# Performance work log

Hardware: AMD Instinct MI355X
Metric: run time of the kernel (lower is better)

## Reference

```python
import jax, jax.numpy as jnp
import numpy as np

N_NODES = 20000
N_EDGES = 500000


def setup_inputs() -> dict:
    key = jax.random.key(0)
    ks = jax.random.split(key, 12)
    s = 0.05  # small init scale for numerical sanity
    return {
        "z": jax.random.normal(ks[0], (N_NODES, 64), jnp.float32),
        "edge_index": jax.random.randint(ks[1], (2, N_EDGES), 0, N_NODES, jnp.int64),
        "celline_feats": jax.random.normal(ks[2], (N_NODES, 4), jnp.float32),
        "esm_repr": jax.random.normal(ks[3], (N_NODES, 320), jnp.float32),
        "mlp_w1": jax.random.normal(ks[4], (4, 64), jnp.float32) * s,
        "mlp_b1": jnp.zeros((64,), jnp.float32),
        "mlp_w2": jax.random.normal(ks[5], (64, 32), jnp.float32) * s,
        "mlp_b2": jnp.zeros((32,), jnp.float32),
        "mlp_w3": jax.random.normal(ks[6], (32, 16), jnp.float32) * s,
        "mlp_b3": jnp.zeros((16,), jnp.float32),
        "fc1_w": jax.random.normal(ks[7], (800, 400), jnp.float32) * s,
        "fc1_b": jnp.zeros((400,), jnp.float32),
        "fc2_w": jax.random.normal(ks[8], (400, 200), jnp.float32) * s,
        "fc2_b": jnp.zeros((200,), jnp.float32),
        "fc3_w": jax.random.normal(ks[9], (200, 100), jnp.float32) * s,
        "fc3_b": jnp.zeros((100,), jnp.float32),
        "fc4_w": jax.random.normal(ks[10], (100, 1), jnp.float32) * s,
        "fc4_b": jnp.zeros((1,), jnp.float32),
    }


def reference(z, edge_index, celline_feats, esm_repr,
              mlp_w1, mlp_b1, mlp_w2, mlp_b2, mlp_w3, mlp_b3,
              fc1_w, fc1_b, fc2_w, fc2_b, fc3_w, fc3_b, fc4_w, fc4_b):
    # cell_line_spec_mlp: 4 -> 64 -> 32 -> 16 (relu, relu, linear)
    m = jax.nn.relu(celline_feats @ mlp_w1 + mlp_b1)
    m = jax.nn.relu(m @ mlp_w2 + mlp_b2)
    m = m @ mlp_w3 + mlp_b3                       # [N, 16]
    # augment node embeddings: [N, 64+16+320] = [N, 400]
    zc = jnp.concatenate([z, m, esm_repr], axis=1)
    # gather endpoints, concat pair features: [E, 800]
    x = jnp.concatenate([zc[edge_index[0]], zc[edge_index[1]]], axis=1)
    # classifier MLP (dropout = identity in eval mode)
    x = jax.nn.relu(x @ fc1_w + fc1_b)
    x = jax.nn.relu(x @ fc2_w + fc2_b)
    x = jax.nn.relu(x @ fc3_w + fc3_b)
    x = x @ fc4_w + fc4_b                          # [E, 1]
    return jnp.squeeze(x, axis=-1)                 # [E]
```

## Files before the change

### kernel.cpp

```cpp
#include <hip/hip_runtime.h>


using u16    = unsigned short;
using f16    = _Float16;
using f16x8  = __attribute__((ext_vector_type(8))) f16;
using f32x4  = __attribute__((ext_vector_type(4))) float;
using f32x16 = __attribute__((ext_vector_type(16))) float;
using i32x4  = __attribute__((ext_vector_type(4))) int;

#define NN   20000
#define NNP  20032
#define KD   416
#define NE   500000
#define NEP  500736
#define GRID_E 3912
#define NB   157

#define W1F_ELEMS (50*13*512)
#define W2F_ELEMS (7*26*512)
#define W3F_ELEMS (4*14*512)
#define F4_ELEMS  128
#define PREP_TOT  (W1F_ELEMS + W2F_ELEMS + W3F_ELEMS + F4_ELEMS)

#define ZC_BLOCKS   (NNP / 4)
#define PREP_BLOCKS ((PREP_TOT + 255) / 256)
#define HIST_BLOCKS ((NE + 1023) / 1024)

__device__ __forceinline__ u16 f2h(float f) {
  f16 h = (f16)f;
  return __builtin_bit_cast(u16, h);
}

__device__ __forceinline__ int cvt_pk_f16(float lo, float hi) {
  int r;
  asm("v_cvt_pkrtz_f16_f32 %0, %1, %2" : "=v"(r) : "v"(lo), "v"(hi));
  return r;
}

__device__ __forceinline__ int pk_addrelu(int p, int q) {
  int r;
  asm("v_pk_add_f16 %0, %1, %2\n\t"
      "v_pk_max_f16 %0, %0, 0"
      : "=&v"(r) : "v"(p), "v"(q));
  return r;
}

__device__ __forceinline__ void gl_lds16(const u16* g, u16* l) {
  __builtin_amdgcn_global_load_lds(
      (const __attribute__((address_space(1))) unsigned int*)g,
      (__attribute__((address_space(3))) unsigned int*)l, 16, 0, 0);
}

__global__ __launch_bounds__(256) void prep_fused(
    const float* __restrict__ z, const float* __restrict__ cell,
    const float* __restrict__ esm,
    const float* __restrict__ w1, const float* __restrict__ b1,
    const float* __restrict__ w2, const float* __restrict__ b2,
    const float* __restrict__ w3, const float* __restrict__ b3,
    u16* __restrict__ zc,
    const float* __restrict__ fc1, const float* __restrict__ fc1b,
    const float* __restrict__ fc2, const float* __restrict__ fc2b,
    const float* __restrict__ fc3, const float* __restrict__ fc3b,
    const float* __restrict__ fc4,
    u16* __restrict__ W1f, u16* __restrict__ W2f, u16* __restrict__ W3f,
    float* __restrict__ fc4wp,
    const int* __restrict__ ei, int* __restrict__ hist)
{
  __shared__ float h1s[4][64];
  __shared__ float h2s[4][32];
  __shared__ float ms[4][16];
  __shared__ int lh[NB];

  if (blockIdx.x < ZC_BLOCKS) {
    int tid = threadIdx.x, g = tid >> 6, t = tid & 63;
    int i = blockIdx.x * 4 + g;
    bool real = (i < NN);
    float c0 = 0, c1 = 0, c2 = 0, c3 = 0;
    if (real) {
      c0 = cell[(size_t)i * 4 + 0]; c1 = cell[(size_t)i * 4 + 1];
      c2 = cell[(size_t)i * 4 + 2]; c3 = cell[(size_t)i * 4 + 3];
    }
    float h = b1[t] + c0 * w1[t] + c1 * w1[64 + t] + c2 * w1[128 + t] + c3 * w1[192 + t];
    h1s[g][t] = fmaxf(h, 0.f);
    __syncthreads();
    if (t < 32) {
      float acc = b2[t];
      #pragma unroll 8
      for (int j = 0; j < 64; j++) acc += h1s[g][j] * w2[j * 32 + t];
      h2s[g][t] = fmaxf(acc, 0.f);
    }
    __syncthreads();
    if (t < 16) {
      float acc = b3[t];
      #pragma unroll 8
      for (int j = 0; j < 32; j++) acc += h2s[g][j] * w3[j * 16 + t];
      ms[g][t] = acc;
    }
    __syncthreads();
    u16* row = zc + (size_t)i * KD;
    for (int k = t; k < KD; k += 64) {
      float v = 0.f;
      if (real) {
        if (k < 64)       v = z[(size_t)i * 64 + k];
        else if (k < 80)  v = ms[g][k - 64];
        else if (k < 400) v = esm[(size_t)i * 320 + (k - 80)];
        else if (k == 400) v = 1.0f;
      }
      row[k] = f2h(v);
    }
    return;
  }

  if (blockIdx.x >= ZC_BLOCKS + PREP_BLOCKS) {
    int tid = threadIdx.x;
    int base = (blockIdx.x - (ZC_BLOCKS + PREP_BLOCKS)) * 1024;
    for (int i = tid; i < NB; i += 256) lh[i] = 0;
    __syncthreads();
    #pragma unroll
    for (int k = 0; k < 4; k++) {
      int e = base + k * 256 + tid;
      if (e < NE) atomicAdd(&lh[ei[e] >> 7], 1);
    }
    __syncthreads();
    for (int i = tid; i < NB; i += 256)
      if (lh[i]) atomicAdd(&hist[i], lh[i]);
    return;
  }

  int idx = (blockIdx.x - ZC_BLOCKS) * 256 + threadIdx.x;
  if (idx < W1F_ELEMS) {
    int j = idx & 7, l = (idx >> 3) & 63, t = idx >> 9;
    int kb = t % 13, g = t / 13;
    int n = g * 16 + (l & 15);
    int k = kb * 32 + (l >> 4) * 8 + j;
    float v = 0.f;
    if (k < 400) v = (n < 400) ? fc1[(size_t)k * 400 + n]
                               : fc1[(size_t)(400 + k) * 400 + (n - 400)];
    else if (k == 400 && n < 400) v = fc1b[n];
    W1f[idx] = f2h(v);
  } else if (idx < W1F_ELEMS + W2F_ELEMS) {
    int r = idx - W1F_ELEMS;
    int j = r & 7, l = (r >> 3) & 63, t = r >> 9;
    int kb = t % 26, nt = t / 26;
    int n = nt * 32 + (l & 31);
    int k = kb * 16 + (l >> 5) * 8 + j;
    float v = 0.f;
    if (n < 200) {
      if (k < 400) v = fc2[(size_t)k * 200 + n];
      else if (k == 400) v = fc2b[n];
    }
    W2f[r] = f2h(v);
  } else if (idx < W1F_ELEMS + W2F_ELEMS + W3F_ELEMS) {
    int r = idx - (W1F_ELEMS + W2F_ELEMS);
    int j = r & 7, l = (r >> 3) & 63, t = r >> 9;
    int kb = t % 14, nt = t / 14;
    int n = nt * 32 + (l & 31);
    int k = kb * 16 + (l >> 5) * 8 + j;
    float v = 0.f;
    if (n < 100) {
      if (k < 200) v = fc3[(size_t)k * 100 + n];
      else if (k == 200) v = fc3b[n];
    }
    W3f[r] = f2h(v);
  } else if (idx < PREP_TOT) {
    int r = idx - (W1F_ELEMS + W2F_ELEMS + W3F_ELEMS);
    fc4wp[r] = (r < 100) ? fc4[r] : 0.f;
  }
}

__global__ __launch_bounds__(256) void scan_pad(
    const int* __restrict__ hist, int* __restrict__ cursor,
    int* __restrict__ sq, int* __restrict__ dq, int* __restrict__ oq)
{
  __shared__ int h[NB];
  __shared__ int cs[NB];
  int t = threadIdx.x;
  if (t < NB) h[t] = hist[t];
  __syncthreads();
  if (t == 0) {
    int run = 0;
    for (int b = 0; b < NB; b++) { cs[b] = run; run += h[b]; }
  }
  __syncthreads();
  if (t < NB) cursor[t] = cs[t];
  for (int i = NE + t; i < NEP; i += 256) {
    sq[i] = 0; dq[i] = 0; oq[i] = 0x7FFFFFFF;
  }
}

__global__ __launch_bounds__(256) void scatter_edges(
    const int* __restrict__ ei, int* __restrict__ cursor,
    int* __restrict__ sq, int* __restrict__ dq, int* __restrict__ oq)
{
  __shared__ int lh[NB];
  __shared__ int lb[NB];
  int t = threadIdx.x;
  int base = blockIdx.x * 1024;
  for (int i = t; i < NB; i += 256) lh[i] = 0;
  __syncthreads();
  int sv[4], dv[4], bv[4], rv[4];
  bool val[4];
  #pragma unroll
  for (int k = 0; k < 4; k++) {
    int e = base + k * 256 + t;
    val[k] = (e < NE);
    if (val[k]) {
      sv[k] = ei[e]; dv[k] = ei[NE + e];
      bv[k] = sv[k] >> 7;
      rv[k] = atomicAdd(&lh[bv[k]], 1);
    }
  }
  __syncthreads();
  for (int i = t; i < NB; i += 256)
    lb[i] = lh[i] ? atomicAdd(&cursor[i], lh[i]) : 0;
  __syncthreads();
  #pragma unroll
  for (int k = 0; k < 4; k++) {
    if (val[k]) {
      int pos = lb[bv[k]] + rv[k];
      sq[pos] = sv[k]; dq[pos] = dv[k]; oq[pos] = base + k * 256 + t;
    }
  }
}

__global__ __launch_bounds__(256) void node_gemm(
    const u16* __restrict__ zc, const u16* __restrict__ W1f,
    u16* __restrict__ PQ)
{
  int tid = threadIdx.x, w = tid >> 6, l = tid & 63, lm = l & 15, quad = l >> 4;
  int mbase = blockIdx.x * 128 + w * 32;

  int ra = mbase + lm;       if (ra > NNP - 1) ra = NNP - 1;
  int rb = mbase + 16 + lm;  if (rb > NNP - 1) rb = NNP - 1;
  f16x8 a0[13], a1[13];
  const u16* arow0 = zc + (size_t)ra * KD + quad * 8;
  const u16* arow1 = zc + (size_t)rb * KD + quad * 8;
  #pragma unroll
  for (int kb = 0; kb < 13; kb++) {
    a0[kb] = *(const f16x8*)(arow0 + kb * 32);
    a1[kb] = *(const f16x8*)(arow1 + kb * 32);
  }

  for (int nt = 0; nt < 10; nt++) {
    int g = blockIdx.y * 10 + nt;
    int ncol = g * 16 + lm;
    const u16* bbase = W1f + ((size_t)g * 13 * 64 + l) * 8;
    f32x4 acc0 = {0.f, 0.f, 0.f, 0.f};
    f32x4 acc1 = {0.f, 0.f, 0.f, 0.f};
    #pragma unroll
    for (int kb = 0; kb < 13; kb++) {
      f16x8 b = *(const f16x8*)(bbase + (size_t)kb * 512);
      acc0 = __builtin_amdgcn_mfma_f32_16x16x32_f16(a0[kb], b, acc0, 0, 0, 0);
      acc1 = __builtin_amdgcn_mfma_f32_16x16x32_f16(a1[kb], b, acc1, 0, 0, 0);
    }
    #pragma unroll
    for (int r = 0; r < 4; r++) {
      int row0 = mbase + quad * 4 + r;
      int row1 = row0 + 16;
      if (row0 < NNP) PQ[(size_t)row0 * 800 + ncol] = f2h(acc0[r]);
      if (row1 < NNP) PQ[(size_t)row1 * 800 + ncol] = f2h(acc1[r]);
    }
  }
}

__global__ __launch_bounds__(256, 2) void edge_kernel(
    const u16* __restrict__ PQ, const u16* __restrict__ W2f,
    const u16* __restrict__ W3f, const float* __restrict__ fc4wp,
    const float* __restrict__ fc4b,
    const int* __restrict__ sq, const int* __restrict__ dq,
    const int* __restrict__ oq, float* __restrict__ out)
{
  __shared__ __align__(16) u16 wsm[2][26 * 512];

  int tid = threadIdx.x, w = tid >> 6, l = tid & 63;
  int c = l & 31, h = l >> 5;
  int bid = blockIdx.x;
  int idx = (bid & 7) * (GRID_E / 8) + (bid >> 3);
  int e = idx * 128 + w * 32 + c;
  int s = sq[e], d = dq[e], oi = oq[e];
  const u16* prow = PQ + (size_t)s * 800 + h * 8;
  const u16* qrow = PQ + (size_t)d * 800 + 400 + h * 8;

  for (int kb = w; kb < 26; kb += 4)
    gl_lds16(W2f + ((size_t)kb * 64 + l) * 8, &wsm[0][kb * 512]);

  i32x4 h1i[25];
  #pragma unroll
  for (int kb = 0; kb < 25; kb++) {
    i32x4 pv = *(const i32x4*)(prow + kb * 16);
    i32x4 qv = *(const i32x4*)(qrow + kb * 16);
    i32x4 r;
    #pragma unroll
    for (int j2 = 0; j2 < 4; j2++) r[j2] = pk_addrelu(pv[j2], qv[j2]);
    h1i[kb] = r;
  }
  i32x4 bias1 = {0, 0, 0, 0};
  if (h == 0) bias1[0] = 0x3C00;

  __syncthreads();

  int p2[7][8];
  #pragma unroll
  for (int nt = 0; nt < 7; nt++) {
    int cur = nt & 1;
    if (nt < 6) {
      for (int kb = w; kb < 26; kb += 4)
        gl_lds16(W2f + (((size_t)(nt + 1) * 26 + kb) * 64 + l) * 8,
                 &wsm[cur ^ 1][kb * 512]);
    } else {
      for (int kb = w; kb < 13; kb += 4)
        gl_lds16(W3f + ((size_t)kb * 64 + l) * 8, &wsm[cur ^ 1][kb * 512]);
    }
    f32x16 acc = {0.f,0.f,0.f,0.f,0.f,0.f,0.f,0.f,0.f,0.f,0.f,0.f,0.f,0.f,0.f,0.f};
    __builtin_amdgcn_s_setprio(1);
    #pragma unroll
    for (int kb = 0; kb < 25; kb++) {
      f16x8 a = *(const f16x8*)&wsm[cur][kb * 512 + l * 8];
      acc = __builtin_amdgcn_mfma_f32_32x32x16_f16(
          a, __builtin_bit_cast(f16x8, h1i[kb]), acc, 0, 0, 0);
    }
    {
      f16x8 a = *(const f16x8*)&wsm[cur][25 * 512 + l * 8];
      acc = __builtin_amdgcn_mfma_f32_32x32x16_f16(
          a, __builtin_bit_cast(f16x8, bias1), acc, 0, 0, 0);
    }
    __builtin_amdgcn_s_setprio(0);
    #pragma unroll
    for (int q = 0; q < 8; q++)
      p2[nt][q] = cvt_pk_f16(fmaxf(acc[2 * q], 0.f), fmaxf(acc[2 * q + 1], 0.f));
    __syncthreads();
  }

  i32x4 b2f[13];
  #pragma unroll
  for (int kb3 = 0; kb3 < 13; kb3++) {
    int nt = kb3 >> 1;
    i32x4 f;
    #pragma unroll
    for (int jj = 0; jj < 4; jj++) {
      int q0 = (jj & 1) + 4 * (kb3 & 1);
      if (jj < 2) {
        int x = __shfl_xor(p2[nt][q0 + 2], 32);
        f[jj] = h ? x : p2[nt][q0];
      } else {
        int y = __shfl_xor(p2[nt][q0], 32);
        f[jj] = h ? p2[nt][q0 + 2] : y;
      }
    }
    if (kb3 == 12 && h) f[0] |= 0x3C00;
    b2f[kb3] = f;
  }

  float osum = 0.f;
  #pragma unroll
  for (int nt3 = 0; nt3 < 4; nt3++) {
    int cur = (7 + nt3) & 1;
    if (nt3 < 3) {
      for (int kb = w; kb < 13; kb += 4)
        gl_lds16(W3f + (((size_t)(nt3 + 1) * 14 + kb) * 64 + l) * 8,
                 &wsm[cur ^ 1][kb * 512]);
    }
    f32x16 acc = {0.f,0.f,0.f,0.f,0.f,0.f,0.f,0.f,0.f,0.f,0.f,0.f,0.f,0.f,0.f,0.f};
    __builtin_amdgcn_s_setprio(1);
    #pragma unroll
    for (int kb3 = 0; kb3 < 13; kb3++) {
      f16x8 a = *(const f16x8*)&wsm[cur][kb3 * 512 + l * 8];
      acc = __builtin_amdgcn_mfma_f32_32x32x16_f16(
          a, __builtin_bit_cast(f16x8, b2f[kb3]), acc, 0, 0, 0);
    }
    __builtin_amdgcn_s_setprio(0);
    #pragma unroll
    for (int r = 0; r < 16; r++) {
      int rho = (r & 3) + 8 * (r >> 2) + 4 * h + 32 * nt3;
      osum += fmaxf(acc[r], 0.f) * fc4wp[rho];
    }
    if (nt3 < 3) __syncthreads();
  }
  osum += __shfl_xor(osum, 32);
  if (h == 0 && oi < NE) out[oi] = osum + fc4b[0];
}

extern "C" void kernel_launch(void* const* d_in, const int* in_sizes, int n_in,
                              void* d_out, int out_size, void* d_ws, size_t ws_size,
                              hipStream_t stream) {
  (void)in_sizes; (void)n_in; (void)out_size; (void)ws_size;
  const float* z    = (const float*)d_in[0];
  const int*   ei   = (const int*)d_in[1];
  const float* cell = (const float*)d_in[2];
  const float* esm  = (const float*)d_in[3];
  const float* w1   = (const float*)d_in[4];
  const float* b1   = (const float*)d_in[5];
  const float* w2   = (const float*)d_in[6];
  const float* b2   = (const float*)d_in[7];
  const float* w3   = (const float*)d_in[8];
  const float* b3   = (const float*)d_in[9];
  const float* fc1w = (const float*)d_in[10];
  const float* fc1b = (const float*)d_in[11];
  const float* fc2w = (const float*)d_in[12];
  const float* fc2b = (const float*)d_in[13];
  const float* fc3w = (const float*)d_in[14];
  const float* fc3b = (const float*)d_in[15];
  const float* fc4w = (const float*)d_in[16];
  const float* fc4b = (const float*)d_in[17];
  float* out = (float*)d_out;

  u16* zc  = (u16*)d_ws;
  u16* PQ  = zc  + (size_t)NNP * KD;
  u16* W1f = PQ  + (size_t)NNP * 800;
  u16* W2f = W1f + W1F_ELEMS;
  u16* W3f = W2f + W2F_ELEMS;
  float* fc4wp = (float*)(W3f + W3F_ELEMS);
  int* hist   = (int*)(fc4wp + 128);
  int* cursor = hist + 160;
  int* sq     = cursor + 160;
  int* dq     = sq + NEP;
  int* oq     = dq + NEP;

  hipMemsetAsync(hist, 0, NB * sizeof(int), stream);
  prep_fused<<<ZC_BLOCKS + PREP_BLOCKS + HIST_BLOCKS, 256, 0, stream>>>(
      z, cell, esm, w1, b1, w2, b2, w3, b3, zc,
      fc1w, fc1b, fc2w, fc2b, fc3w, fc3b, fc4w, W1f, W2f, W3f, fc4wp,
      ei, hist);
  scan_pad<<<1, 256, 0, stream>>>(hist, cursor, sq, dq, oq);
  scatter_edges<<<HIST_BLOCKS, 256, 0, stream>>>(ei, cursor, sq, dq, oq);
  node_gemm<<<dim3((NNP + 127) / 128, 5), 256, 0, stream>>>(zc, W1f, PQ);
  edge_kernel<<<GRID_E, 256, 0, stream>>>(PQ, W2f, W3f, fc4wp, fc4b,
                                          sq, dq, oq, out);
}
```

Measured before the change: 370.2 us.

## Split edge-kernel weight staging into half-tile double buffers to halve LDS

Weight tiles for the fc2 and fc3 layers are now staged in halves of the K dimension rather than whole tiles. The double buffer shrinks from two 26-block slots to two 13-block slots. Each output tile computes its first half from one buffer while the second half loads, then swaps after a mid-tile barrier. This halves shared-memory use, which could allow more resident blocks, at the cost of an extra __syncthreads per tile and a shorter window for hiding loads.

Measured after the change: 378.9 us. 2.3% more time.

```diff
diff --git a/kernel.cpp b/kernel.cpp
--- a/kernel.cpp
+++ b/kernel.cpp
@@ -263,6 +263,34 @@
   }
 }
 
+
+#define STAGE2(nt, hf, b) \
+  for (int kb = w; kb < 13; kb += 4) \
+    gl_lds16(W2f + (((size_t)(nt) * 26 + (hf) * 13 + kb) * 64 + l) * 8, \
+             &wsm[b][kb * 512]);
+
+#define STAGE3(nt, hf, b) \
+  for (int kb = w; kb < ((hf) ? 6 : 7); kb += 4) \
+    gl_lds16(W3f + (((size_t)(nt) * 14 + (hf) * 7 + kb) * 64 + l) * 8, \
+             &wsm[b][kb * 512]);
+
+#define FC2_HALF(hf, b) \
+  _Pragma("unroll") \
+  for (int kk = 0; kk < 13; kk++) { \
+    int gkb = (hf) * 13 + kk; \
+    f16x8 a = *(const f16x8*)&wsm[b][kk * 512 + l * 8]; \
+    acc = __builtin_amdgcn_mfma_f32_32x32x16_f16( \
+        a, __builtin_bit_cast(f16x8, gkb < 25 ? h1i[gkb] : bias1), acc, 0, 0, 0); \
+  }
+
+#define FC3_HALF(hf, b) \
+  _Pragma("unroll") \
+  for (int kk = 0; kk < ((hf) ? 6 : 7); kk++) { \
+    f16x8 a = *(const f16x8*)&wsm[b][kk * 512 + l * 8]; \
+    acc = __builtin_amdgcn_mfma_f32_32x32x16_f16( \
+        a, __builtin_bit_cast(f16x8, b2f[(hf) * 7 + kk]), acc, 0, 0, 0); \
+  }
+
 __global__ __launch_bounds__(256, 2) void edge_kernel(
     const u16* __restrict__ PQ, const u16* __restrict__ W2f,
     const u16* __restrict__ W3f, const float* __restrict__ fc4wp,
@@ -270,7 +298,7 @@
     const int* __restrict__ sq, const int* __restrict__ dq,
     const int* __restrict__ oq, float* __restrict__ out)
 {
-  __shared__ __align__(16) u16 wsm[2][26 * 512];
+  __shared__ __align__(16) u16 wsm[2][13 * 512];
 
   int tid = threadIdx.x, w = tid >> 6, l = tid & 63;
   int c = l & 31, h = l >> 5;
@@ -281,8 +309,7 @@
   const u16* prow = PQ + (size_t)s * 800 + h * 8;
   const u16* qrow = PQ + (size_t)d * 800 + 400 + h * 8;
 
-  for (int kb = w; kb < 26; kb += 4)
-    gl_lds16(W2f + ((size_t)kb * 64 + l) * 8, &wsm[0][kb * 512]);
+  STAGE2(0, 0, 0);
 
   i32x4 h1i[25];
   #pragma unroll
@@ -302,28 +329,16 @@
   int p2[7][8];
   #pragma unroll
   for (int nt = 0; nt < 7; nt++) {
-    int cur = nt & 1;
-    if (nt < 6) {
-      for (int kb = w; kb < 26; kb += 4)
-        gl_lds16(W2f + (((size_t)(nt + 1) * 26 + kb) * 64 + l) * 8,
-                 &wsm[cur ^ 1][kb * 512]);
-    } else {
-      for (int kb = w; kb < 13; kb += 4)
-        gl_lds16(W3f + ((size_t)kb * 64 + l) * 8, &wsm[cur ^ 1][kb * 512]);
-    }
+    STAGE2(nt, 1, 1);
     f32x16 acc = {0.f,0.f,0.f,0.f,0.f,0.f,0.f,0.f,0.f,0.f,0.f,0.f,0.f,0.f,0.f,0.f};
     __builtin_amdgcn_s_setprio(1);
-    #pragma unroll
-    for (int kb = 0; kb < 25; kb++) {
-      f16x8 a = *(const f16x8*)&wsm[cur][kb * 512 + l * 8];
-      acc = __builtin_amdgcn_mfma_f32_32x32x16_f16(
-          a, __builtin_bit_cast(f16x8, h1i[kb]), acc, 0, 0, 0);
-    }
-    {
-      f16x8 a = *(const f16x8*)&wsm[cur][25 * 512 + l * 8];
-      acc = __builtin_amdgcn_mfma_f32_32x32x16_f16(
-          a, __builtin_bit_cast(f16x8, bias1), acc, 0, 0, 0);
-    }
+    FC2_HALF(0, 0);
+    __builtin_amdgcn_s_setprio(0);
+    __syncthreads();
+    if (nt < 6) { STAGE2(nt + 1, 0, 0); }
+    else        { STAGE3(0, 0, 0); }
+    __builtin_amdgcn_s_setprio(1);
+    FC2_HALF(1, 1);
     __builtin_amdgcn_s_setprio(0);
     #pragma unroll
     for (int q = 0; q < 8; q++)
@@ -354,20 +369,15 @@
   float osum = 0.f;
   #pragma unroll
   for (int nt3 = 0; nt3 < 4; nt3++) {
-    int cur = (7 + nt3) & 1;
-    if (nt3 < 3) {
-      for (int kb = w; kb < 13; kb += 4)
-        gl_lds16(W3f + (((size_t)(nt3 + 1) * 14 + kb) * 64 + l) * 8,
-                 &wsm[cur ^ 1][kb * 512]);
-    }
+    STAGE3(nt3, 1, 1);
     f32x16 acc = {0.f,0.f,0.f,0.f,0.f,0.f,0.f,0.f,0.f,0.f,0.f,0.f,0.f,0.f,0.f,0.f};
     __builtin_amdgcn_s_setprio(1);
-    #pragma unroll
-    for (int kb3 = 0; kb3 < 13; kb3++) {
-      f16x8 a = *(const f16x8*)&wsm[cur][kb3 * 512 + l * 8];
-      acc = __builtin_amdgcn_mfma_f32_32x32x16_f16(
-          a, __builtin_bit_cast(f16x8, b2f[kb3]), acc, 0, 0, 0);
-    }
+    FC3_HALF(0, 0);
+    __builtin_amdgcn_s_setprio(0);
+    __syncthreads();
+    if (nt3 < 3) { STAGE3(nt3 + 1, 0, 0); }
+    __builtin_amdgcn_s_setprio(1);
+    FC3_HALF(1, 1);
     __builtin_amdgcn_s_setprio(0);
     #pragma unroll
     for (int r = 0; r < 16; r++) {
```

## Bucket edges by 2D source/destination node blocks for gather locality

Applied to the files above, without the earlier changes.

Edges were bucketed by source block only (157 buckets). They are now bucketed by the (source block, destination block) pair, giving 157x157 buckets. The goal is to make the per-edge gathers of PQ rows in the edge kernel hit a small working set of both source and destination nodes, improving cache reuse. In exchange the histogram and scatter use global atomics directly, with no shared-memory aggregation, which adds contention. A single block now scans about 24.6K buckets serially per thread, and the workspace grows.

Result: slower. 433.5 us (+17.1%).

```diff
diff --git a/kernel.cpp b/kernel.cpp
--- a/kernel.cpp
+++ b/kernel.cpp
@@ -14,7 +14,8 @@
 #define NE   500000
 #define NEP  500736
 #define GRID_E 3912
-#define NB   157
+#define NBS  157
+#define NB2  (157*157)
 
 #define W1F_ELEMS (50*13*512)
 #define W2F_ELEMS (7*26*512)
@@ -69,7 +70,6 @@
   __shared__ float h1s[4][64];
   __shared__ float h2s[4][32];
   __shared__ float ms[4][16];
-  __shared__ int lh[NB];
 
   if (blockIdx.x < ZC_BLOCKS) {
     int tid = threadIdx.x, g = tid >> 6, t = tid & 63;
@@ -114,16 +114,14 @@
   if (blockIdx.x >= ZC_BLOCKS + PREP_BLOCKS) {
     int tid = threadIdx.x;
     int base = (blockIdx.x - (ZC_BLOCKS + PREP_BLOCKS)) * 1024;
-    for (int i = tid; i < NB; i += 256) lh[i] = 0;
-    __syncthreads();
     #pragma unroll
     for (int k = 0; k < 4; k++) {
       int e = base + k * 256 + tid;
-      if (e < NE) atomicAdd(&lh[ei[e] >> 7], 1);
-    }
-    __syncthreads();
-    for (int i = tid; i < NB; i += 256)
-      if (lh[i]) atomicAdd(&hist[i], lh[i]);
+      if (e < NE) {
+        int s = ei[e], d = ei[NE + e];
+        atomicAdd(&hist[(s >> 7) * NBS + (d >> 7)], 1);
+      }
+    }
     return;
   }
 
@@ -172,17 +170,21 @@
     const int* __restrict__ hist, int* __restrict__ cursor,
     int* __restrict__ sq, int* __restrict__ dq, int* __restrict__ oq)
 {
-  __shared__ int h[NB];
-  __shared__ int cs[NB];
+  __shared__ int part[256];
   int t = threadIdx.x;
-  if (t < NB) h[t] = hist[t];
+  const int per = (NB2 + 255) / 256;
+  int lo = t * per, hi = lo + per; if (hi > NB2) hi = NB2;
+  int sum = 0;
+  for (int i = lo; i < hi; i++) sum += hist[i];
+  part[t] = sum;
   __syncthreads();
   if (t == 0) {
     int run = 0;
-    for (int b = 0; b < NB; b++) { cs[b] = run; run += h[b]; }
+    for (int i = 0; i < 256; i++) { int v = part[i]; part[i] = run; run += v; }
   }
   __syncthreads();
-  if (t < NB) cursor[t] = cs[t];
+  int run = part[t];
+  for (int i = lo; i < hi; i++) { int v = hist[i]; cursor[i] = run; run += v; }
   for (int i = NE + t; i < NEP; i += 256) {
     sq[i] = 0; dq[i] = 0; oq[i] = 0x7FFFFFFF;
   }
@@ -192,33 +194,16 @@
     const int* __restrict__ ei, int* __restrict__ cursor,
     int* __restrict__ sq, int* __restrict__ dq, int* __restrict__ oq)
 {
-  __shared__ int lh[NB];
-  __shared__ int lb[NB];
   int t = threadIdx.x;
   int base = blockIdx.x * 1024;
-  for (int i = t; i < NB; i += 256) lh[i] = 0;
-  __syncthreads();
-  int sv[4], dv[4], bv[4], rv[4];
-  bool val[4];
   #pragma unroll
   for (int k = 0; k < 4; k++) {
     int e = base + k * 256 + t;
-    val[k] = (e < NE);
-    if (val[k]) {
-      sv[k] = ei[e]; dv[k] = ei[NE + e];
-      bv[k] = sv[k] >> 7;
-      rv[k] = atomicAdd(&lh[bv[k]], 1);
-    }
-  }
-  __syncthreads();
-  for (int i = t; i < NB; i += 256)
-    lb[i] = lh[i] ? atomicAdd(&cursor[i], lh[i]) : 0;
-  __syncthreads();
-  #pragma unroll
-  for (int k = 0; k < 4; k++) {
-    if (val[k]) {
-      int pos = lb[bv[k]] + rv[k];
-      sq[pos] = sv[k]; dq[pos] = dv[k]; oq[pos] = base + k * 256 + t;
+    if (e < NE) {
+      int s = ei[e], d = ei[NE + e];
+      int key = (s >> 7) * NBS + (d >> 7);
+      int pos = atomicAdd(&cursor[key], 1);
+      sq[pos] = s; dq[pos] = d; oq[pos] = e;
     }
   }
 }
@@ -411,12 +396,12 @@
   u16* W3f = W2f + W2F_ELEMS;
   float* fc4wp = (float*)(W3f + W3F_ELEMS);
   int* hist   = (int*)(fc4wp + 128);
-  int* cursor = hist + 160;
-  int* sq     = cursor + 160;
+  int* cursor = hist + NB2;
+  int* sq     = cursor + NB2;
   int* dq     = sq + NEP;
   int* oq     = dq + NEP;
 
-  hipMemsetAsync(hist, 0, NB * sizeof(int), stream);
+  hipMemsetAsync(hist, 0, NB2 * sizeof(int), stream);
   prep_fused<<<ZC_BLOCKS + PREP_BLOCKS + HIST_BLOCKS, 256, 0, stream>>>(
       z, cell, esm, w1, b1, w2, b2, w3, b3, zc,
       fc1w, fc1b, fc2w, fc2b, fc3w, fc3b, fc4w, W1f, W2f, W3f, fc4wp,
```
